# Performance work log

Measured on AMD Instinct MI355X. Metric: run time of the kernel, lower is better.

Reference implementation:

```python
import jax, jax.numpy as jnp
import numpy as np

HEADS = 2

def gat_layer(x, edge_index, W, att, bias):
    # x: [N, Fin], W: [H*C, Fin], att: [1, H, 2C], bias: [C]
    N = x.shape[0]
    C = bias.shape[0]
    # add self loops (source_to_target: x_j from row 0, aggregate onto row 1)
    loop = jnp.arange(N, dtype=edge_index.dtype)
    src = jnp.concatenate([edge_index[0], loop])
    dst = jnp.concatenate([edge_index[1], loop])
    h = (x @ W.T).reshape(N, HEADS, C)          # [N, H, C]
    x_j = h[src]                                 # [E, H, C]
    x_i = h[dst]                                 # [E, H, C]
    x_cat = jnp.concatenate([x_i, x_j], axis=-1) # [E, H, 2C]
    alpha = (x_cat * att).sum(-1)                # [E, H]
    alpha = jnp.where(alpha >= 0, alpha, 0.2 * alpha)  # leaky_relu(0.2)
    # NOTE: module uses a global (not per-destination) normalization
    alpha = jnp.exp(alpha - alpha.max())
    alpha = alpha / (alpha.sum(axis=0, keepdims=True) + 1e-10)
    msg = x_j * alpha[..., None]                 # [E, H, C]
    aggr = jax.ops.segment_sum(msg, dst, num_segments=N)  # [N, H, C]
    return aggr.mean(axis=1) + bias              # [N, C]

def setup_inputs() -> dict:
    key = jax.random.key(0)
    ks = jax.random.split(key, 7)
    N, Fin, C = 50000, 128, 64
    E = 800000
    x = jax.random.normal(ks[0], (N, Fin), dtype=jnp.float32)
    edge_index = jax.random.randint(ks[1], (2, E), 0, N, dtype=jnp.int64)
    W1 = jax.random.normal(ks[2], (HEADS * C, Fin), dtype=jnp.float32) * 0.05
    att1 = jax.random.normal(ks[3], (1, HEADS, 2 * C), dtype=jnp.float32) * 0.05
    b1 = jnp.zeros((C,), dtype=jnp.float32)
    W2 = jax.random.normal(ks[4], (HEADS * C, C), dtype=jnp.float32) * 0.05
    att2 = jax.random.normal(ks[5], (1, HEADS, 2 * C), dtype=jnp.float32) * 0.05
    b2 = jnp.zeros((C,), dtype=jnp.float32)
    return {"x": x, "edge_index": edge_index, "W1": W1, "att1": att1,
            "b1": b1, "W2": W2, "att2": att2, "b2": b2}

def reference(x, edge_index, W1, att1, b1, W2, att2, b2):
    h = gat_layer(x, edge_index, W1, att1, b1)
    h = jax.nn.relu(h)
    # F.dropout with training flag: treated as eval (identity) for determinism
    out = gat_layer(h, edge_index, W2, att2, b2)
    return out
```

## Files before the change

kernel.cpp:

```cpp
#include <hip/hip_runtime.h>
#include <hip/hip_bf16.h>
#include <math.h>


#define HP 8
#define HG 64
#define NHISTB (HP * HG)
#define HRANGE_MAX 6272
#define NZ    256
#define NWGT  512

using short8 = __attribute__((ext_vector_type(8))) short;
using f32x4  = __attribute__((ext_vector_type(4))) float;

__device__ __forceinline__ unsigned f2bf(float x) {
  unsigned u = __float_as_uint(x);
  return (u + 0x7fffu + ((u >> 16) & 1u)) >> 16;
}
__device__ __forceinline__ float bflo(unsigned p) { return __uint_as_float(p << 16); }
__device__ __forceinline__ float bfhi(unsigned p) { return __uint_as_float(p & 0xffff0000u); }
__device__ __forceinline__ float lrexp(float a) {
  a = a >= 0.f ? a : 0.2f * a;
  return __expf(a);
}

__global__ __launch_bounds__(256) void init_ws(
    const float* __restrict__ W1, const float* __restrict__ W2,
    unsigned short* __restrict__ wbf1, unsigned short* __restrict__ wbf2,
    float* __restrict__ Z) {
  int tid = blockIdx.x * 256 + threadIdx.x;
  int stride = gridDim.x * 256;
  for (int i = tid; i < 128 * 128; i += stride)
    wbf1[i] = (unsigned short)f2bf(W1[i]);
  for (int i = tid; i < 128 * 64; i += stride)
    wbf2[i] = (unsigned short)f2bf(W2[i]);
  if (tid < 4) Z[tid] = 0.f;
}

template <int FIN>
__global__ __launch_bounds__(256) void gemm_mfma(
    const float* __restrict__ x, const unsigned short* __restrict__ Wb,
    const float* __restrict__ att, unsigned* __restrict__ hq,
    float* __restrict__ si, float* __restrict__ sj,
    int N,
    const int* __restrict__ dstE, int* __restrict__ partial,
    int E, int nhistb, int hstep) {
  const int tid = threadIdx.x;

  constexpr int WB = 128 * FIN * 2;
  constexpr int SMEM = (WB > HRANGE_MAX * 4) ? WB : HRANGE_MAX * 4;
  __shared__ __align__(16) unsigned char smem[SMEM];

  if ((int)blockIdx.x < nhistb) {
    int* lhist = (int*)smem;
    const int p = blockIdx.x & (HP - 1);
    const int g = blockIdx.x >> 3;
    const int lo = p * hstep;
    for (int i = tid; i < hstep; i += 256) lhist[i] = 0;
    __syncthreads();
    const int stride = HG * 256;
    int e = g * 256 + tid;
    for (; e + 3 * stride < E; e += 4 * stride) {
      int d0 = dstE[e] - lo;
      int d1 = dstE[e + stride] - lo;
      int d2 = dstE[e + 2 * stride] - lo;
      int d3 = dstE[e + 3 * stride] - lo;
      if ((unsigned)d0 < (unsigned)hstep) atomicAdd(&lhist[d0], 1);
      if ((unsigned)d1 < (unsigned)hstep) atomicAdd(&lhist[d1], 1);
      if ((unsigned)d2 < (unsigned)hstep) atomicAdd(&lhist[d2], 1);
      if ((unsigned)d3 < (unsigned)hstep) atomicAdd(&lhist[d3], 1);
    }
    for (; e < E; e += stride) {
      int d = dstE[e] - lo;
      if ((unsigned)d < (unsigned)hstep) atomicAdd(&lhist[d], 1);
    }
    __syncthreads();
    for (int i = tid; i < hstep; i += 256) {
      int node = lo + i;
      if (node < N) partial[(size_t)g * N + node] = lhist[i];
    }
    return;
  }

  constexpr int KS = FIN / 32;
  constexpr int CPR = FIN / 8;
  constexpr int NCHUNK = 128 * CPR;

  unsigned short* wlds = (unsigned short*)smem;

  const int w    = tid >> 6;
  const int lane = tid & 63;
  const int cl   = lane & 15;
  const int grp  = lane >> 4;
  const int n0   = (blockIdx.x - nhistb) * 64;

  const int arow = n0 + w * 16 + cl;
  const bool avalid = arow < N;
  float4 av0[KS], av1[KS];
#pragma unroll
  for (int ks = 0; ks < KS; ++ks) {
    av0[ks] = make_float4(0.f, 0.f, 0.f, 0.f);
    av1[ks] = av0[ks];
    if (avalid) {
      const float4* xp =
          (const float4*)(x + (size_t)arow * FIN + ks * 32 + grp * 8);
      av0[ks] = xp[0];
      av1[ks] = xp[1];
    }
  }

  const uint4* Wb4 = (const uint4*)Wb;
  for (int c = tid; c < NCHUNK; c += 256) {
    int row = c / CPR;
    int cc  = c & (CPR - 1);
    *(uint4*)&wlds[row * FIN + ((cc ^ (row & (CPR - 1))) * 8)] = Wb4[c];
  }
  __syncthreads();

  short8 afrag[KS];
#pragma unroll
  for (int ks = 0; ks < KS; ++ks) {
    union { short8 s8; unsigned u[4]; } af;
    af.u[0] = f2bf(av0[ks].x) | (f2bf(av0[ks].y) << 16);
    af.u[1] = f2bf(av0[ks].z) | (f2bf(av0[ks].w) << 16);
    af.u[2] = f2bf(av1[ks].x) | (f2bf(av1[ks].y) << 16);
    af.u[3] = f2bf(av1[ks].z) | (f2bf(av1[ks].w) << 16);
    afrag[ks] = af.s8;
  }

  f32x4 acc[8];
#pragma unroll
  for (int ct = 0; ct < 8; ++ct) acc[ct] = (f32x4){0.f, 0.f, 0.f, 0.f};

  const int swz = cl & (CPR - 1);
#pragma unroll
  for (int ks = 0; ks < KS; ++ks) {
#pragma unroll
    for (int ct = 0; ct < 8; ++ct) {
      const unsigned short* bp =
          &wlds[(ct * 16 + cl) * FIN + (((ks * 4 + grp) ^ swz) * 8)];
      short8 bfrag = *(const short8*)bp;
      acc[ct] = __builtin_amdgcn_mfma_f32_16x16x32_bf16(afrag[ks], bfrag,
                                                        acc[ct], 0, 0, 0);
    }
  }

  float ai[8], aj[8];
#pragma unroll
  for (int ct = 0; ct < 8; ++ct) {
    int hd = ct >> 2;
    int cw = (ct & 3) * 16 + cl;
    ai[ct] = att[hd * 128 + cw];
    aj[ct] = att[hd * 128 + 64 + cw];
  }

#pragma unroll
  for (int r = 0; r < 4; ++r) {
    int node = n0 + w * 16 + grp * 4 + r;
    float s0i = 0.f, s0j = 0.f, s1i = 0.f, s1j = 0.f;
    unsigned wpk[4];
#pragma unroll
    for (int ct = 0; ct < 4; ++ct) {
      float v0 = acc[ct][r];
      float v1 = acc[ct + 4][r];
      s0i += v0 * ai[ct];
      s0j += v0 * aj[ct];
      s1i += v1 * ai[ct + 4];
      s1j += v1 * aj[ct + 4];
      wpk[ct] = f2bf(v0) | (f2bf(v1) << 16);
    }
#pragma unroll
    for (int off = 8; off; off >>= 1) {
      s0i += __shfl_xor(s0i, off, 64);
      s0j += __shfl_xor(s0j, off, 64);
      s1i += __shfl_xor(s1i, off, 64);
      s1j += __shfl_xor(s1j, off, 64);
    }
    if (node < N) {
#pragma unroll
      for (int ct = 0; ct < 4; ++ct)
        hq[(size_t)node * 64 + ct * 16 + cl] = wpk[ct];
      if (cl == 0) {
        si[node * 2 + 0] = s0i;
        si[node * 2 + 1] = s1i;
        sj[node * 2 + 0] = s0j;
        sj[node * 2 + 1] = s1j;
      }
    }
  }
}

__device__ __forceinline__ void z_edge_body(
    const int* __restrict__ srcE, const int* __restrict__ dstE,
    const float2* __restrict__ si2, const float2* __restrict__ sj2,
    float* __restrict__ Zp, int E, int Etot, int tid0, int stride) {
  float z0 = 0.f, z1 = 0.f;
  for (int e = tid0; e < Etot; e += stride) {
    int s, d;
    if (e < E) { s = srcE[e]; d = dstE[e]; } else { s = d = e - E; }
    float2 siv = si2[d];
    float2 sjv = sj2[s];
    z0 += lrexp(siv.x + sjv.x);
    z1 += lrexp(siv.y + sjv.y);
  }
  __shared__ float r0[4], r1[4];
  int lane = threadIdx.x & 63, w = threadIdx.x >> 6;
#pragma unroll
  for (int off = 32; off; off >>= 1) {
    z0 += __shfl_down(z0, off, 64);
    z1 += __shfl_down(z1, off, 64);
  }
  if (lane == 0) { r0[w] = z0; r1[w] = z1; }
  __syncthreads();
  if (threadIdx.x == 0) {
    atomicAdd(&Zp[0], r0[0] + r0[1] + r0[2] + r0[3]);
    atomicAdd(&Zp[1], r1[0] + r1[1] + r1[2] + r1[3]);
  }
}

__global__ __launch_bounds__(256) void z_edge_wgt(
    const int* __restrict__ srcE, const int* __restrict__ dstE,
    const float2* __restrict__ si2, const float2* __restrict__ sj2,
    float* __restrict__ Zp, float4* __restrict__ erec, int E, int Etot) {
  if ((int)blockIdx.x < NZ) {
    z_edge_body(srcE, dstE, si2, sj2, Zp, E, Etot,
                blockIdx.x * 256 + threadIdx.x, NZ * 256);
    return;
  }
  int k = (blockIdx.x - NZ) * 256 + threadIdx.x;
  int stride = NWGT * 256;
  for (; k < E; k += stride) {
    float4 r = erec[k];
    int s = __float_as_int(r.x);
    int d = __float_as_int(r.y);
    float2 siv = si2[d];
    float2 sjv = sj2[s];
    r.z = lrexp(siv.x + sjv.x);
    r.w = lrexp(siv.y + sjv.y);
    erec[k] = r;
  }
}

__global__ __launch_bounds__(256) void scan_blocks(
    const int* __restrict__ partial, int* __restrict__ rowptr,
    int* __restrict__ bsum, int N) {
  __shared__ int ts[256];
  int b = blockIdx.x, t = threadIdx.x;
  int base = b * 1024 + t * 4;
  int s0 = 0, s1 = 0, s2 = 0, s3 = 0;
  if (base < N) {
    const int4* p4 = (const int4*)partial;
#pragma unroll 4
    for (int g = 0; g < HG; ++g) {
      int4 v = p4[((size_t)g * N + base) >> 2];
      s0 += v.x; s1 += v.y; s2 += v.z; s3 += v.w;
    }
  }
  int v[4] = {s0, s1, s2, s3};
  int tot = s0 + s1 + s2 + s3;
  ts[t] = tot;
  __syncthreads();
#pragma unroll
  for (int off = 1; off < 256; off <<= 1) {
    int x = (t >= off) ? ts[t - off] : 0;
    __syncthreads();
    ts[t] += x;
    __syncthreads();
  }
  int run = ts[t] - tot;
#pragma unroll
  for (int j = 0; j < 4; ++j) {
    if (base + j < N) rowptr[base + j] = run;
    run += v[j];
  }
  if (t == 255) bsum[b] = ts[255];
}

__global__ __launch_bounds__(256) void scan_finish(
    int* __restrict__ rowptr, const int* __restrict__ bsum,
    int* __restrict__ partial, int N, int Eall, int nb) {
  __shared__ int pre[256];
  if (threadIdx.x == 0) {
    int run = 0;
    for (int i = 0; i < nb; ++i) { pre[i] = run; run += bsum[i]; }
  }
  __syncthreads();
  int tid = blockIdx.x * blockDim.x + threadIdx.x;
  int stride = gridDim.x * blockDim.x;
  for (int i = tid; i < N; i += stride) {
    int v = rowptr[i] + pre[i >> 10];
    rowptr[i] = v;
    int run = v;
#pragma unroll 8
    for (int g = 0; g < HG; ++g) {
      int c = partial[(size_t)g * N + i];
      partial[(size_t)g * N + i] = run;
      run += c;
    }
  }
  if (tid == 0) rowptr[N] = Eall;
}

__global__ __launch_bounds__(256) void scatter_z(
    const int* __restrict__ srcE, const int* __restrict__ dstE,
    const int* __restrict__ partial, float4* __restrict__ erec,
    const float2* __restrict__ si2, const float2* __restrict__ sj2,
    float* __restrict__ Zp, int E, int Etot, int hstep, int N) {
  __shared__ __align__(16) int lcur[HRANGE_MAX];
  if ((int)blockIdx.x < NZ) {
    z_edge_body(srcE, dstE, si2, sj2, Zp, E, Etot,
                blockIdx.x * 256 + threadIdx.x, NZ * 256);
    return;
  }
  const int bid = blockIdx.x - NZ;
  const int p = bid & (HP - 1);
  const int g = bid >> 3;
  const int lo = p * hstep;
  const int tid = threadIdx.x;
  for (int i = tid; i < hstep; i += 256) {
    int node = lo + i;
    lcur[i] = (node < N) ? partial[(size_t)g * N + node] : 0;
  }
  __syncthreads();
  const int stride = HG * 256;
  int e = g * 256 + tid;
  for (; e + 3 * stride < E; e += 4 * stride) {
    int d0 = dstE[e], d1 = dstE[e + stride];
    int d2 = dstE[e + 2 * stride], d3 = dstE[e + 3 * stride];
    int t0 = d0 - lo, t1 = d1 - lo, t2 = d2 - lo, t3 = d3 - lo;
    if ((unsigned)t0 < (unsigned)hstep) {
      int s = srcE[e];
      float2 siv = si2[d0], sjv = sj2[s];
      erec[atomicAdd(&lcur[t0], 1)] = make_float4(
          __int_as_float(s), __int_as_float(d0),
          lrexp(siv.x + sjv.x), lrexp(siv.y + sjv.y));
    }
    if ((unsigned)t1 < (unsigned)hstep) {
      int s = srcE[e + stride];
      float2 siv = si2[d1], sjv = sj2[s];
      erec[atomicAdd(&lcur[t1], 1)] = make_float4(
          __int_as_float(s), __int_as_float(d1),
          lrexp(siv.x + sjv.x), lrexp(siv.y + sjv.y));
    }
    if ((unsigned)t2 < (unsigned)hstep) {
      int s = srcE[e + 2 * stride];
      float2 siv = si2[d2], sjv = sj2[s];
      erec[atomicAdd(&lcur[t2], 1)] = make_float4(
          __int_as_float(s), __int_as_float(d2),
          lrexp(siv.x + sjv.x), lrexp(siv.y + sjv.y));
    }
    if ((unsigned)t3 < (unsigned)hstep) {
      int s = srcE[e + 3 * stride];
      float2 siv = si2[d3], sjv = sj2[s];
      erec[atomicAdd(&lcur[t3], 1)] = make_float4(
          __int_as_float(s), __int_as_float(d3),
          lrexp(siv.x + sjv.x), lrexp(siv.y + sjv.y));
    }
  }
  for (; e < E; e += stride) {
    int d = dstE[e];
    int dd = d - lo;
    if ((unsigned)dd < (unsigned)hstep) {
      int s = srcE[e];
      float2 siv = si2[d], sjv = sj2[s];
      erec[atomicAdd(&lcur[dd], 1)] = make_float4(
          __int_as_float(s), __int_as_float(d),
          lrexp(siv.x + sjv.x), lrexp(siv.y + sjv.y));
    }
  }
}

__device__ __forceinline__ void edge4r(
    const float4* __restrict__ erec, int k, const unsigned* __restrict__ hq,
    int lane, float& acc0, float& acc1) {
  float4 r0 = erec[k], r1 = erec[k + 1], r2 = erec[k + 2], r3 = erec[k + 3];
  unsigned p0 = hq[(size_t)__float_as_int(r0.x) * 64 + lane];
  unsigned p1 = hq[(size_t)__float_as_int(r1.x) * 64 + lane];
  unsigned p2 = hq[(size_t)__float_as_int(r2.x) * 64 + lane];
  unsigned p3 = hq[(size_t)__float_as_int(r3.x) * 64 + lane];
  acc0 = fmaf(bflo(p0), r0.z, acc0);
  acc1 = fmaf(bfhi(p0), r0.w, acc1);
  acc0 = fmaf(bflo(p1), r1.z, acc0);
  acc1 = fmaf(bfhi(p1), r1.w, acc1);
  acc0 = fmaf(bflo(p2), r2.z, acc0);
  acc1 = fmaf(bfhi(p2), r2.w, acc1);
  acc0 = fmaf(bflo(p3), r3.z, acc0);
  acc1 = fmaf(bfhi(p3), r3.w, acc1);
}
__device__ __forceinline__ void edge1r(
    int s, float w0, float w1, const unsigned* __restrict__ hq, int lane,
    float& acc0, float& acc1) {
  unsigned p = hq[(size_t)s * 64 + lane];
  acc0 = fmaf(bflo(p), w0, acc0);
  acc1 = fmaf(bfhi(p), w1, acc1);
}

__global__ __launch_bounds__(256) void csr_aggregate(
    const int* __restrict__ rowptr, const float4* __restrict__ erec,
    const unsigned* __restrict__ hq, const float2* __restrict__ si2,
    const float2* __restrict__ sj2, const float* __restrict__ Zp,
    const float* __restrict__ bias, float* __restrict__ out,
    int N, int do_relu) {
  int lane = threadIdx.x & 63;
  int wid = (blockIdx.x * blockDim.x + threadIdx.x) >> 6;
  int nw = (gridDim.x * blockDim.x) >> 6;
  float z0 = 1.f / (Zp[0] + 1e-10f);
  float z1 = 1.f / (Zp[1] + 1e-10f);
  float bv = bias[lane];
  for (int n0 = wid; n0 < N; n0 += nw) {
    int n = __builtin_amdgcn_readfirstlane(n0);
    int beg = rowptr[n], end = rowptr[n + 1];
    float2 siv = si2[n];
    float2 jv = sj2[n];
    float acc0 = 0.f, acc1 = 0.f;
    edge1r(n, lrexp(siv.x + jv.x), lrexp(siv.y + jv.y), hq, lane, acc0, acc1);
    int k = beg;
    for (; k + 4 <= end; k += 4) edge4r(erec, k, hq, lane, acc0, acc1);
    for (; k < end; ++k) {
      float4 r = erec[k];
      edge1r(__float_as_int(r.x), r.z, r.w, hq, lane, acc0, acc1);
    }
    float r = 0.5f * (acc0 * z0 + acc1 * z1) + bv;
    if (do_relu) r = fmaxf(r, 0.f);
    out[(size_t)n * 64 + lane] = r;
  }
}

extern "C" void kernel_launch(void* const* d_in, const int* in_sizes, int n_in,
                              void* d_out, int out_size, void* d_ws, size_t ws_size,
                              hipStream_t stream) {
  const float* x    = (const float*)d_in[0];
  const int*   ei   = (const int*)d_in[1];
  const float* W1   = (const float*)d_in[2];
  const float* att1 = (const float*)d_in[3];
  const float* b1   = (const float*)d_in[4];
  const float* W2   = (const float*)d_in[5];
  const float* att2 = (const float*)d_in[6];
  const float* b2   = (const float*)d_in[7];
  float* out = (float*)d_out;

  const int N = in_sizes[0] / 128;
  const int E = in_sizes[1] / 2;
  const int Etot = E + N;
  const int* srcE = ei;
  const int* dstE = ei + E;

  unsigned* hq = (unsigned*)d_ws;
  float* si    = (float*)(hq + (size_t)N * 64);
  float* sj    = si + (size_t)N * 2;
  float* Z     = sj + (size_t)N * 2;
  float* x2    = Z + 4;
  int* partial = (int*)x2;
  int* rowptr  = (int*)(x2 + (size_t)N * 64);
  int* bsum    = rowptr + (N + 1);
  uintptr_t ep = ((uintptr_t)(bsum + 256) + 15) & ~(uintptr_t)15;
  float4* erec = (float4*)ep;
  unsigned short* wbf1 = (unsigned short*)(erec + E);
  unsigned short* wbf2 = wbf1 + 128 * 128;

  dim3 blk(256);
  int nb = (N + 1023) / 1024;
  int ntiles = (N + 63) / 64;
  int hstep = (N + HP - 1) / HP;

  init_ws<<<64, blk, 0, stream>>>(W1, W2, wbf1, wbf2, Z);
  gemm_mfma<128><<<NHISTB + ntiles, blk, 0, stream>>>(
      x, wbf1, att1, hq, si, sj, N, dstE, partial, E, NHISTB, hstep);
  scan_blocks<<<nb, blk, 0, stream>>>(partial, rowptr, bsum, N);
  scan_finish<<<256, blk, 0, stream>>>(rowptr, bsum, partial, N, E, nb);
  scatter_z<<<NZ + NHISTB, blk, 0, stream>>>(
      srcE, dstE, partial, erec, (const float2*)si, (const float2*)sj,
      Z, E, Etot, hstep, N);
  csr_aggregate<<<4096, blk, 0, stream>>>(rowptr, erec, hq,
                                          (const float2*)si, (const float2*)sj,
                                          Z, b1, x2, N, 1);
  gemm_mfma<64><<<ntiles, blk, 0, stream>>>(
      x2, wbf2, att2, hq, si, sj, N, dstE, partial, E, 0, hstep);
  z_edge_wgt<<<NZ + NWGT, blk, 0, stream>>>(
      srcE, dstE, (const float2*)si, (const float2*)sj, Z + 2, erec, E, Etot);
  csr_aggregate<<<4096, blk, 0, stream>>>(rowptr, erec, hq,
                                          (const float2*)si, (const float2*)sj,
                                          Z + 2, b2, out, N, 0);
}
```

Baseline: 279.3 us.

## Fuse softmax denominator into edge scatter and weight passes, chunk edges contiguously

The separate Z-reduction pass over all edges is removed. Z is now accumulated inside the scatter kernel for layer 1 and inside the weight-recompute kernel for layer 2, with a few extra blocks covering the self-loop terms. This avoids re-reading the edge lists and the si/sj gathers a second time. The histogram and scatter blocks now handle contiguous edge chunks instead of strided ones, and scatter and z_wgt2 run with 1024-thread blocks. The cost is that floating-point summation order changes, and the large blocks may lower occupancy.

```diff
diff --git a/kernel.cpp b/kernel.cpp
--- a/kernel.cpp
+++ b/kernel.cpp
@@ -7,8 +7,8 @@
 #define HG 64
 #define NHISTB (HP * HG)
 #define HRANGE_MAX 6272
-#define NZ    256
-#define NWGT  512
+#define NSELF 16
+#define NWGT  256
 
 using short8 = __attribute__((ext_vector_type(8))) short;
 using f32x4  = __attribute__((ext_vector_type(4))) float;
@@ -22,6 +22,26 @@
 __device__ __forceinline__ float lrexp(float a) {
   a = a >= 0.f ? a : 0.2f * a;
   return __expf(a);
+}
+
+__device__ __forceinline__ void block_zadd(float z0, float z1,
+                                           float* __restrict__ Zp) {
+  __shared__ float r0[16], r1[16];
+  int lane = threadIdx.x & 63, w = threadIdx.x >> 6;
+  int nw = blockDim.x >> 6;
+#pragma unroll
+  for (int off = 32; off; off >>= 1) {
+    z0 += __shfl_down(z0, off, 64);
+    z1 += __shfl_down(z1, off, 64);
+  }
+  if (lane == 0) { r0[w] = z0; r1[w] = z1; }
+  __syncthreads();
+  if (threadIdx.x == 0) {
+    float s0 = 0.f, s1 = 0.f;
+    for (int i = 0; i < nw; ++i) { s0 += r0[i]; s1 += r1[i]; }
+    atomicAdd(&Zp[0], s0);
+    atomicAdd(&Zp[1], s1);
+  }
 }
 
 __global__ __launch_bounds__(256) void init_ws(
@@ -44,7 +64,7 @@
     float* __restrict__ si, float* __restrict__ sj,
     int N,
     const int* __restrict__ dstE, int* __restrict__ partial,
-    int E, int nhistb, int hstep) {
+    int E, int nhistb, int hstep, int eper) {
   const int tid = threadIdx.x;
 
   constexpr int WB = 128 * FIN * 2;
@@ -58,19 +78,20 @@
     const int lo = p * hstep;
     for (int i = tid; i < hstep; i += 256) lhist[i] = 0;
     __syncthreads();
-    const int stride = HG * 256;
-    int e = g * 256 + tid;
-    for (; e + 3 * stride < E; e += 4 * stride) {
+    const int eb = g * eper;
+    const int ee = min(E, eb + eper);
+    int e = eb + tid;
+    for (; e + 3 * 256 < ee; e += 4 * 256) {
       int d0 = dstE[e] - lo;
-      int d1 = dstE[e + stride] - lo;
-      int d2 = dstE[e + 2 * stride] - lo;
-      int d3 = dstE[e + 3 * stride] - lo;
+      int d1 = dstE[e + 256] - lo;
+      int d2 = dstE[e + 2 * 256] - lo;
+      int d3 = dstE[e + 3 * 256] - lo;
       if ((unsigned)d0 < (unsigned)hstep) atomicAdd(&lhist[d0], 1);
       if ((unsigned)d1 < (unsigned)hstep) atomicAdd(&lhist[d1], 1);
       if ((unsigned)d2 < (unsigned)hstep) atomicAdd(&lhist[d2], 1);
       if ((unsigned)d3 < (unsigned)hstep) atomicAdd(&lhist[d3], 1);
     }
-    for (; e < E; e += stride) {
+    for (; e < ee; e += 256) {
       int d = dstE[e] - lo;
       if ((unsigned)d < (unsigned)hstep) atomicAdd(&lhist[d], 1);
     }
@@ -187,57 +208,6 @@
         sj[node * 2 + 1] = s1j;
       }
     }
-  }
-}
-
-__device__ __forceinline__ void z_edge_body(
-    const int* __restrict__ srcE, const int* __restrict__ dstE,
-    const float2* __restrict__ si2, const float2* __restrict__ sj2,
-    float* __restrict__ Zp, int E, int Etot, int tid0, int stride) {
-  float z0 = 0.f, z1 = 0.f;
-  for (int e = tid0; e < Etot; e += stride) {
-    int s, d;
-    if (e < E) { s = srcE[e]; d = dstE[e]; } else { s = d = e - E; }
-    float2 siv = si2[d];
-    float2 sjv = sj2[s];
-    z0 += lrexp(siv.x + sjv.x);
-    z1 += lrexp(siv.y + sjv.y);
-  }
-  __shared__ float r0[4], r1[4];
-  int lane = threadIdx.x & 63, w = threadIdx.x >> 6;
-#pragma unroll
-  for (int off = 32; off; off >>= 1) {
-    z0 += __shfl_down(z0, off, 64);
-    z1 += __shfl_down(z1, off, 64);
-  }
-  if (lane == 0) { r0[w] = z0; r1[w] = z1; }
-  __syncthreads();
-  if (threadIdx.x == 0) {
-    atomicAdd(&Zp[0], r0[0] + r0[1] + r0[2] + r0[3]);
-    atomicAdd(&Zp[1], r1[0] + r1[1] + r1[2] + r1[3]);
-  }
-}
-
-__global__ __launch_bounds__(256) void z_edge_wgt(
-    const int* __restrict__ srcE, const int* __restrict__ dstE,
-    const float2* __restrict__ si2, const float2* __restrict__ sj2,
-    float* __restrict__ Zp, float4* __restrict__ erec, int E, int Etot) {
-  if ((int)blockIdx.x < NZ) {
-    z_edge_body(srcE, dstE, si2, sj2, Zp, E, Etot,
-                blockIdx.x * 256 + threadIdx.x, NZ * 256);
-    return;
-  }
-  int k = (blockIdx.x - NZ) * 256 + threadIdx.x;
-  int stride = NWGT * 256;
-  for (; k < E; k += stride) {
-    float4 r = erec[k];
-    int s = __float_as_int(r.x);
-    int d = __float_as_int(r.y);
-    float2 siv = si2[d];
-    float2 sjv = sj2[s];
-    r.z = lrexp(siv.x + sjv.x);
-    r.w = lrexp(siv.y + sjv.y);
-    erec[k] = r;
   }
 }
 
@@ -301,73 +271,114 @@
   if (tid == 0) rowptr[N] = Eall;
 }
 
-__global__ __launch_bounds__(256) void scatter_z(
+__global__ __launch_bounds__(1024) void scatter_z(
     const int* __restrict__ srcE, const int* __restrict__ dstE,
     const int* __restrict__ partial, float4* __restrict__ erec,
     const float2* __restrict__ si2, const float2* __restrict__ sj2,
-    float* __restrict__ Zp, int E, int Etot, int hstep, int N) {
+    float* __restrict__ Zp, int E, int hstep, int N, int eper) {
   __shared__ __align__(16) int lcur[HRANGE_MAX];
-  if ((int)blockIdx.x < NZ) {
-    z_edge_body(srcE, dstE, si2, sj2, Zp, E, Etot,
-                blockIdx.x * 256 + threadIdx.x, NZ * 256);
+  const int tid = threadIdx.x;
+  float z0 = 0.f, z1 = 0.f;
+
+  if ((int)blockIdx.x < NSELF) {
+    for (int n = blockIdx.x * 1024 + tid; n < N; n += NSELF * 1024) {
+      float2 a = si2[n], b = sj2[n];
+      z0 += lrexp(a.x + b.x);
+      z1 += lrexp(a.y + b.y);
+    }
+    block_zadd(z0, z1, Zp);
     return;
   }
-  const int bid = blockIdx.x - NZ;
+
+  const int bid = blockIdx.x - NSELF;
   const int p = bid & (HP - 1);
   const int g = bid >> 3;
   const int lo = p * hstep;
-  const int tid = threadIdx.x;
-  for (int i = tid; i < hstep; i += 256) {
+  for (int i = tid; i < hstep; i += 1024) {
     int node = lo + i;
     lcur[i] = (node < N) ? partial[(size_t)g * N + node] : 0;
   }
   __syncthreads();
-  const int stride = HG * 256;
-  int e = g * 256 + tid;
-  for (; e + 3 * stride < E; e += 4 * stride) {
-    int d0 = dstE[e], d1 = dstE[e + stride];
-    int d2 = dstE[e + 2 * stride], d3 = dstE[e + 3 * stride];
+
+  const int eb = g * eper;
+  const int ee = min(E, eb + eper);
+  int e = eb + tid;
+  for (; e + 3 * 1024 < ee; e += 4 * 1024) {
+    int d0 = dstE[e], d1 = dstE[e + 1024];
+    int d2 = dstE[e + 2 * 1024], d3 = dstE[e + 3 * 1024];
+    int s0 = srcE[e], s1 = srcE[e + 1024];
+    int s2 = srcE[e + 2 * 1024], s3 = srcE[e + 3 * 1024];
     int t0 = d0 - lo, t1 = d1 - lo, t2 = d2 - lo, t3 = d3 - lo;
     if ((unsigned)t0 < (unsigned)hstep) {
-      int s = srcE[e];
-      float2 siv = si2[d0], sjv = sj2[s];
-      erec[atomicAdd(&lcur[t0], 1)] = make_float4(
-          __int_as_float(s), __int_as_float(d0),
-          lrexp(siv.x + sjv.x), lrexp(siv.y + sjv.y));
+      float2 siv = si2[d0], sjv = sj2[s0];
+      float w0 = lrexp(siv.x + sjv.x), w1 = lrexp(siv.y + sjv.y);
+      z0 += w0; z1 += w1;
+      erec[atomicAdd(&lcur[t0], 1)] =
+          make_float4(__int_as_float(s0), __int_as_float(d0), w0, w1);
     }
     if ((unsigned)t1 < (unsigned)hstep) {
-      int s = srcE[e + stride];
-      float2 siv = si2[d1], sjv = sj2[s];
-      erec[atomicAdd(&lcur[t1], 1)] = make_float4(
-          __int_as_float(s), __int_as_float(d1),
-          lrexp(siv.x + sjv.x), lrexp(siv.y + sjv.y));
+      float2 siv = si2[d1], sjv = sj2[s1];
+      float w0 = lrexp(siv.x + sjv.x), w1 = lrexp(siv.y + sjv.y);
+      z0 += w0; z1 += w1;
+      erec[atomicAdd(&lcur[t1], 1)] =
+          make_float4(__int_as_float(s1), __int_as_float(d1), w0, w1);
     }
     if ((unsigned)t2 < (unsigned)hstep) {
-      int s = srcE[e + 2 * stride];
-      float2 siv = si2[d2], sjv = sj2[s];
-      erec[atomicAdd(&lcur[t2], 1)] = make_float4(
-          __int_as_float(s), __int_as_float(d2),
-          lrexp(siv.x + sjv.x), lrexp(siv.y + sjv.y));
+      float2 siv = si2[d2], sjv = sj2[s2];
+      float w0 = lrexp(siv.x + sjv.x), w1 = lrexp(siv.y + sjv.y);
+      z0 += w0; z1 += w1;
+      erec[atomicAdd(&lcur[t2], 1)] =
+          make_float4(__int_as_float(s2), __int_as_float(d2), w0, w1);
     }
     if ((unsigned)t3 < (unsigned)hstep) {
-      int s = srcE[e + 3 * stride];
-      float2 siv = si2[d3], sjv = sj2[s];
-      erec[atomicAdd(&lcur[t3], 1)] = make_float4(
-          __int_as_float(s), __int_as_float(d3),
-          lrexp(siv.x + sjv.x), lrexp(siv.y + sjv.y));
-    }
-  }
-  for (; e < E; e += stride) {
+      float2 siv = si2[d3], sjv = sj2[s3];
+      float w0 = lrexp(siv.x + sjv.x), w1 = lrexp(siv.y + sjv.y);
+      z0 += w0; z1 += w1;
+      erec[atomicAdd(&lcur[t3], 1)] =
+          make_float4(__int_as_float(s3), __int_as_float(d3), w0, w1);
+    }
+  }
+  for (; e < ee; e += 1024) {
     int d = dstE[e];
     int dd = d - lo;
     if ((unsigned)dd < (unsigned)hstep) {
       int s = srcE[e];
       float2 siv = si2[d], sjv = sj2[s];
-      erec[atomicAdd(&lcur[dd], 1)] = make_float4(
-          __int_as_float(s), __int_as_float(d),
-          lrexp(siv.x + sjv.x), lrexp(siv.y + sjv.y));
-    }
-  }
+      float w0 = lrexp(siv.x + sjv.x), w1 = lrexp(siv.y + sjv.y);
+      z0 += w0; z1 += w1;
+      erec[atomicAdd(&lcur[dd], 1)] =
+          make_float4(__int_as_float(s), __int_as_float(d), w0, w1);
+    }
+  }
+  block_zadd(z0, z1, Zp);
+}
+
+__global__ __launch_bounds__(1024) void z_wgt2(
+    const float2* __restrict__ si2, const float2* __restrict__ sj2,
+    float* __restrict__ Zp, float4* __restrict__ erec, int E, int N) {
+  const int tid = threadIdx.x;
+  float z0 = 0.f, z1 = 0.f;
+  if ((int)blockIdx.x < NSELF) {
+    for (int n = blockIdx.x * 1024 + tid; n < N; n += NSELF * 1024) {
+      float2 a = si2[n], b = sj2[n];
+      z0 += lrexp(a.x + b.x);
+      z1 += lrexp(a.y + b.y);
+    }
+  } else {
+    int k = (blockIdx.x - NSELF) * 1024 + tid;
+    for (; k < E; k += NWGT * 1024) {
+      float4 r = erec[k];
+      int s = __float_as_int(r.x);
+      int d = __float_as_int(r.y);
+      float2 siv = si2[d];
+      float2 sjv = sj2[s];
+      r.z = lrexp(siv.x + sjv.x);
+      r.w = lrexp(siv.y + sjv.y);
+      z0 += r.z; z1 += r.w;
+      erec[k] = r;
+    }
+  }
+  block_zadd(z0, z1, Zp);
 }
 
 __device__ __forceinline__ void edge4r(
@@ -441,7 +452,6 @@
 
   const int N = in_sizes[0] / 128;
   const int E = in_sizes[1] / 2;
-  const int Etot = E + N;
   const int* srcE = ei;
   const int* dstE = ei + E;
 
@@ -459,25 +469,27 @@
   unsigned short* wbf2 = wbf1 + 128 * 128;
 
   dim3 blk(256);
+  dim3 blk1k(1024);
   int nb = (N + 1023) / 1024;
   int ntiles = (N + 63) / 64;
   int hstep = (N + HP - 1) / HP;
+  int eper  = (E + HG - 1) / HG;
 
   init_ws<<<64, blk, 0, stream>>>(W1, W2, wbf1, wbf2, Z);
   gemm_mfma<128><<<NHISTB + ntiles, blk, 0, stream>>>(
-      x, wbf1, att1, hq, si, sj, N, dstE, partial, E, NHISTB, hstep);
+      x, wbf1, att1, hq, si, sj, N, dstE, partial, E, NHISTB, hstep, eper);
   scan_blocks<<<nb, blk, 0, stream>>>(partial, rowptr, bsum, N);
   scan_finish<<<256, blk, 0, stream>>>(rowptr, bsum, partial, N, E, nb);
-  scatter_z<<<NZ + NHISTB, blk, 0, stream>>>(
+  scatter_z<<<NSELF + NHISTB, blk1k, 0, stream>>>(
       srcE, dstE, partial, erec, (const float2*)si, (const float2*)sj,
-      Z, E, Etot, hstep, N);
+      Z, E, hstep, N, eper);
   csr_aggregate<<<4096, blk, 0, stream>>>(rowptr, erec, hq,
                                           (const float2*)si, (const float2*)sj,
                                           Z, b1, x2, N, 1);
   gemm_mfma<64><<<ntiles, blk, 0, stream>>>(
-      x2, wbf2, att2, hq, si, sj, N, dstE, partial, E, 0, hstep);
-  z_edge_wgt<<<NZ + NWGT, blk, 0, stream>>>(
-      srcE, dstE, (const float2*)si, (const float2*)sj, Z + 2, erec, E, Etot);
+      x2, wbf2, att2, hq, si, sj, N, dstE, partial, E, 0, hstep, eper);
+  z_wgt2<<<NSELF + NWGT, blk1k, 0, stream>>>(
+      (const float2*)si, (const float2*)sj, Z + 2, erec, E, N);
   csr_aggregate<<<4096, blk, 0, stream>>>(rowptr, erec, hq,
                                           (const float2*)si, (const float2*)sj,
                                           Z + 2, b2, out, N, 0);
```

Measured after the change: 256.3 us. 1.09x faster.
